# Kernel optimization log

Hardware: AMD Instinct MI355X
Metric: run time of the kernel (lower is better)

The kernel has to match this reference:

```python
import jax, jax.numpy as jnp
import numpy as np

D = 1024          # d_model
DFF_S = 2 * D     # memory/router FFN
DFF_E = 8 * D     # expert FFN
B = 1024          # batch
EPS = 1e-5
MEM_IDS = np.array([0, 2, 6, 8])    # corners: 'memory'
SMALL_IDS = np.array([0, 2, 4, 6, 8])  # dim_ff = 2*d (memory + router)
EXP_IDS = np.array([1, 3, 5, 7])    # edges: 'expert', dim_ff = 8*d

def _adjacency():
    A = np.zeros((9, 9), np.float32)
    for r in range(3):
        for c in range(3):
            i = r * 3 + c
            if r > 0: A[i, (r - 1) * 3 + c] = 1.0
            if r < 2: A[i, (r + 1) * 3 + c] = 1.0
            if c > 0: A[i, r * 3 + (c - 1)] = 1.0
            if c < 2: A[i, r * 3 + (c + 1)] = 1.0
    return A

def _ln(x, s, b):
    # x: [9, B, 1, D]; s, b: [9, D] (per-node LayerNorm params)
    mu = jnp.mean(x, axis=-1, keepdims=True)
    var = jnp.mean(jnp.square(x - mu), axis=-1, keepdims=True)
    return (x - mu) * jax.lax.rsqrt(var + EPS) * s[:, None, None, :] + b[:, None, None, :]

def setup_inputs() -> dict:
    key = jax.random.key(0)
    ks = jax.random.split(key, 12)
    sc = 0.02
    inp = {
        'seed': jax.random.normal(ks[0], (B, 1, D), jnp.float32),
        'ln1_s': jnp.ones((9, D), jnp.float32),
        'ln1_b': jnp.zeros((9, D), jnp.float32),
        'v_w': sc * jax.random.normal(ks[1], (9, D, D), jnp.float32),
        'v_b': jnp.zeros((9, D), jnp.float32),
        'o_w': sc * jax.random.normal(ks[2], (9, D, D), jnp.float32),
        'o_b': jnp.zeros((9, D), jnp.float32),
        'ln2_s': jnp.ones((9, D), jnp.float32),
        'ln2_b': jnp.zeros((9, D), jnp.float32),
        'w1_s': sc * jax.random.normal(ks[3], (5, DFF_S, D), jnp.float32),
        'b1_s': jnp.zeros((5, DFF_S), jnp.float32),
        'w2_s': sc * jax.random.normal(ks[4], (5, D, DFF_S), jnp.float32),
        'b2_s': jnp.zeros((5, D), jnp.float32),
        'w1_e': sc * jax.random.normal(ks[5], (4, DFF_E, D), jnp.float32),
        'b1_e': jnp.zeros((4, DFF_E), jnp.float32),
        'w2_e': sc * jax.random.normal(ks[6], (4, D, DFF_E), jnp.float32),
        'b2_e': jnp.zeros((4, D), jnp.float32),
        'steps': 3,
    }
    return inp

def reference(seed, ln1_s, ln1_b, v_w, v_b, o_w, o_b, ln2_s, ln2_b,
              w1_s, b1_s, w2_s, b2_s, w1_e, b1_e, w2_e, b2_e, steps):
    b = seed.shape[0]
    A = jnp.asarray(_adjacency(), seed.dtype)           # [9, 9] static grid topology
    S = jnp.zeros((9, b, 1, D), seed.dtype).at[4].set(seed)  # center = router = seed
    mem = jnp.zeros((4, b, 1, D), seed.dtype)           # memory-node hidden buffers
    mids = jnp.asarray(MEM_IDS)
    sids = jnp.asarray(SMALL_IDS)
    eids = jnp.asarray(EXP_IDS)
    for _ in range(steps):
        # neighbor sum over static 3x3 grid topology
        integ = jnp.einsum('mn,nbtd->mbtd', A, S)
        xn = _ln(integ, ln1_s, ln1_b)
        # seq_len == 1 => softmax over one key is 1 => attn = out_proj(v_proj(xn))
        v = jnp.einsum('nij,nbtj->nbti', v_w, xn) + v_b[:, None, None, :]
        attn = jnp.einsum('nij,nbtj->nbti', o_w, v) + o_b[:, None, None, :]
        x = integ + attn
        # memory nodes: new_memory = 0.7*mem + 0.3*x; x <- new_memory; buffer detached
        new_mem = 0.7 * mem + 0.3 * x[mids]
        x = x.at[mids].set(new_mem)
        mem = jax.lax.stop_gradient(new_mem)
        xn2 = _ln(x, ln2_s, ln2_b)
        # per-role MLPs (ReLU FFN)
        hs = jax.nn.relu(jnp.einsum('nfj,nbtj->nbtf', w1_s, xn2[sids]) + b1_s[:, None, None, :])
        outs = jnp.einsum('njf,nbtf->nbtj', w2_s, hs) + b2_s[:, None, None, :]
        he = jax.nn.relu(jnp.einsum('nfj,nbtj->nbtf', w1_e, xn2[eids]) + b1_e[:, None, None, :])
        oute = jnp.einsum('njf,nbtf->nbtj', w2_e, he) + b2_e[:, None, None, :]
        S = x.at[sids].add(outs).at[eids].add(oute)
    return S  # [9, B, 1, D] = final grid states
```

## Files before the change

### kernel.cpp

```cpp
#include <hip/hip_runtime.h>

#define BD (1024LL * 1024LL)

using bf16x8 = __attribute__((ext_vector_type(8))) __bf16;
using f32x4  = __attribute__((ext_vector_type(4))) float;

__device__ __forceinline__ unsigned short f2bf(float f) {
  unsigned int u = __float_as_uint(f);
  u += 0x7fffu + ((u >> 16) & 1u);
  return (unsigned short)(u >> 16);
}
__device__ __forceinline__ float bf2f(unsigned short h) {
  return __uint_as_float((unsigned int)h << 16);
}

__device__ __forceinline__ void gl_lds16(const unsigned short* g, unsigned short* l) {
  __builtin_amdgcn_global_load_lds(
      (const __attribute__((address_space(1))) void*)g,
      (__attribute__((address_space(3))) void*)l, 16, 0, 0);
}

__global__ __launch_bounds__(256) void cvt_kernel(const float* __restrict__ src,
                                                  unsigned short* __restrict__ dst,
                                                  long long n4) {
  long long i = (long long)blockIdx.x * 256 + threadIdx.x;
  if (i >= n4) return;
  float4 v = *(const float4*)(src + i * 4);
  unsigned int lo = (unsigned int)f2bf(v.x) | ((unsigned int)f2bf(v.y) << 16);
  unsigned int hi = (unsigned int)f2bf(v.z) | ((unsigned int)f2bf(v.w) << 16);
  *(uint2*)(dst + i * 4) = make_uint2(lo, hi);
}

__global__ __launch_bounds__(256) void tcvt_kernel(const float* __restrict__ src,
                                                   unsigned short* __restrict__ dst) {
  __shared__ float tile[32][33];
  const int n = blockIdx.z;
  const int bk = blockIdx.y * 32;
  const int bj = blockIdx.x * 32;
  const int tx = threadIdx.x & 31;
  const int ty = threadIdx.x >> 5;
#pragma unroll
  for (int r = 0; r < 4; ++r)
    tile[ty + r * 8][tx] = src[(long long)n * BD + (long long)(bk + ty + r * 8) * 1024 + bj + tx];
  __syncthreads();
#pragma unroll
  for (int r = 0; r < 4; ++r)
    dst[(long long)n * BD + (long long)(bj + ty + r * 8) * 1024 + bk + tx] =
        f2bf(tile[tx][ty + r * 8]);
}

__global__ __launch_bounds__(256) void cb_kernel(const float* __restrict__ o_w,
                                                 const float* __restrict__ v_b,
                                                 const float* __restrict__ o_b,
                                                 float* __restrict__ cb) {
  const int n = blockIdx.y;
  const int i = blockIdx.x * 4 + (threadIdx.x >> 6);
  const int lane = threadIdx.x & 63;
  const float* row = o_w + (long long)n * BD + (long long)i * 1024;
  const float* vb = v_b + n * 1024;
  float s = 0.f;
#pragma unroll
  for (int t = 0; t < 16; ++t) s += row[lane + t * 64] * vb[lane + t * 64];
  for (int off = 32; off > 0; off >>= 1) s += __shfl_down(s, off);
  if (lane == 0) cb[n * 1024 + i] = o_b[n * 1024 + i] + s;
}

__global__ __launch_bounds__(256) void init_kernel(const float* __restrict__ seed,
                                                   float* __restrict__ S,
                                                   float* __restrict__ mem) {
  long long i = (long long)blockIdx.x * 256 + threadIdx.x;
  const long long S4 = 9 * BD / 4;
  if (i < S4) {
    float4 v = make_float4(0.f, 0.f, 0.f, 0.f);
    const long long lo4 = 4 * BD / 4, hi4 = 5 * BD / 4;
    if (i >= lo4 && i < hi4) v = *(const float4*)(seed + (i - lo4) * 4);
    *(float4*)(S + i * 4) = v;
  } else {
    long long j = i - S4;
    *(float4*)(mem + j * 4) = make_float4(0.f, 0.f, 0.f, 0.f);
  }
}

template <bool ADJ>
__global__ __launch_bounds__(256) void ln_kernel(const float* __restrict__ in,
                                                 const float* __restrict__ gam,
                                                 const float* __restrict__ bet,
                                                 float* __restrict__ integ,
                                                 unsigned short* __restrict__ out) {
  const int row = blockIdx.x;
  const int node = blockIdx.y;
  const int tid = threadIdx.x;
  const long long rowoff = (long long)row * 1024 + tid * 4;
  const long long base = (long long)node * BD + rowoff;
  float4 v;
  if (ADJ) {
    v = make_float4(0.f, 0.f, 0.f, 0.f);
    const int r = node / 3, c = node % 3;
    if (r > 0) { float4 t = *(const float4*)(in + (node - 3) * BD + rowoff); v.x += t.x; v.y += t.y; v.z += t.z; v.w += t.w; }
    if (r < 2) { float4 t = *(const float4*)(in + (node + 3) * BD + rowoff); v.x += t.x; v.y += t.y; v.z += t.z; v.w += t.w; }
    if (c > 0) { float4 t = *(const float4*)(in + (node - 1) * BD + rowoff); v.x += t.x; v.y += t.y; v.z += t.z; v.w += t.w; }
    if (c < 2) { float4 t = *(const float4*)(in + (node + 1) * BD + rowoff); v.x += t.x; v.y += t.y; v.z += t.z; v.w += t.w; }
    *(float4*)(integ + base) = v;
  } else {
    v = *(const float4*)(in + base);
  }
  float s = v.x + v.y + v.z + v.w;
  float q = v.x * v.x + v.y * v.y + v.z * v.z + v.w * v.w;
  for (int off = 32; off > 0; off >>= 1) {
    s += __shfl_down(s, off);
    q += __shfl_down(q, off);
  }
  __shared__ float red[8];
  if ((tid & 63) == 0) { red[tid >> 6] = s; red[4 + (tid >> 6)] = q; }
  __syncthreads();
  s = red[0] + red[1] + red[2] + red[3];
  q = red[4] + red[5] + red[6] + red[7];
  const float mean = s * (1.0f / 1024.0f);
  const float var = q * (1.0f / 1024.0f) - mean * mean;
  const float inv = rsqrtf(var + 1e-5f);
  const float4 g = *(const float4*)(gam + node * 1024 + tid * 4);
  const float4 b = *(const float4*)(bet + node * 1024 + tid * 4);
  const float o0 = (v.x - mean) * inv * g.x + b.x;
  const float o1 = (v.y - mean) * inv * g.y + b.y;
  const float o2 = (v.z - mean) * inv * g.z + b.z;
  const float o3 = (v.w - mean) * inv * g.w + b.w;
  unsigned int lo = (unsigned int)f2bf(o0) | ((unsigned int)f2bf(o1) << 16);
  unsigned int hi = (unsigned int)f2bf(o2) | ((unsigned int)f2bf(o3) << 16);
  *(uint2*)(out + base) = make_uint2(lo, hi);
}

template <int MODE>
__global__ __launch_bounds__(256, 3) void gemm_kernel(
    const unsigned short* __restrict__ X, long long sX,
    const unsigned short* __restrict__ W, long long sW,
    const float* __restrict__ bias, int sBias,
    const float* __restrict__ add, long long sAdd,
    float* __restrict__ memio,
    void* __restrict__ outp, long long sOut,
    int N, int K, int SK) {
  __shared__ unsigned short Als[128 * 32];
  __shared__ unsigned short Bls[128 * 32];
  const int z = blockIdx.z;
  const int node = z / SK;
  const int kz = z - node * SK;
  const int Kper = K / SK;
  const int kbeg = kz * Kper;
  const long long bm = (long long)blockIdx.y * 128;
  const long long bn = (long long)blockIdx.x * 128;
  const unsigned short* Xz = X + (long long)node * sX;
  const unsigned short* Wz = W + (long long)node * sW;
  const int tid = threadIdx.x;
  const int lane = tid & 63;
  const int wid = tid >> 6;
  const int wm = (wid >> 1) * 64;
  const int wn = (wid & 1) * 64;
  const int lm = lane & 15;
  const int quad = lane >> 4;

  f32x4 acc[4][4] = {};

  const int lrow = lane >> 2;
  const int gch = ((lane & 3) ^ ((lane >> 3) & 3)) * 8;
  const int fch = (quad ^ ((lm >> 1) & 3)) * 8;

  for (int k0 = kbeg; k0 < kbeg + Kper; k0 += 32) {
    __syncthreads();
#pragma unroll
    for (int t = 0; t < 2; ++t) {
      const int idx = wid * 2 + t;
      const long long row = idx * 16 + lrow;
      gl_lds16(Xz + (bm + row) * K + k0 + gch, &Als[idx * 512]);
      gl_lds16(Wz + (bn + row) * K + k0 + gch, &Bls[idx * 512]);
    }
    __syncthreads();
    bf16x8 af[4], bfv[4];
#pragma unroll
    for (int i = 0; i < 4; ++i)
      af[i] = *(const bf16x8*)&Als[(wm + i * 16 + lm) * 32 + fch];
#pragma unroll
    for (int j = 0; j < 4; ++j)
      bfv[j] = *(const bf16x8*)&Bls[(wn + j * 16 + lm) * 32 + fch];
#pragma unroll
    for (int i = 0; i < 4; ++i)
#pragma unroll
      for (int j = 0; j < 4; ++j)
        acc[i][j] = __builtin_amdgcn_mfma_f32_16x16x32_bf16(af[i], bfv[j], acc[i][j], 0, 0, 0);
  }

  if (MODE == 4) {
    unsigned short* out = (unsigned short*)outp + (long long)z * sOut;
#pragma unroll
    for (int i = 0; i < 4; ++i) {
      const long long rb = bm + wm + i * 16 + quad * 4;
#pragma unroll
      for (int j = 0; j < 4; ++j) {
        const int col = (int)bn + wn + j * 16 + lm;
#pragma unroll
        for (int r = 0; r < 4; ++r)
          out[(rb + r) * (long long)N + col] = f2bf(acc[i][j][r]);
      }
    }
  } else {
    const float* bz = bias + (long long)node * sBias;
    float* out = (float*)outp + (long long)node * sOut;
    const float* az = add + (long long)node * sAdd;
    const bool is_mem = (node != 4) && ((node & 1) == 0);
    float* mz = nullptr;
    if (is_mem) {
      const int mi = (node == 0) ? 0 : (node == 2) ? 1 : (node == 6) ? 2 : 3;
      mz = memio + (long long)mi * BD;
    }
#pragma unroll
    for (int i = 0; i < 4; ++i) {
      const long long rb = bm + wm + i * 16 + quad * 4;
#pragma unroll
      for (int j = 0; j < 4; ++j) {
        const int col = (int)bn + wn + j * 16 + lm;
        const float bv = bz[col];
#pragma unroll
        for (int r = 0; r < 4; ++r) {
          const long long idx = (rb + r) * (long long)N + col;
          float v = acc[i][j][r] + bv + az[idx];
          if (is_mem) {
            v = 0.7f * mz[idx] + 0.3f * v;
            mz[idx] = v;
          }
          out[idx] = v;
        }
      }
    }
  }
}

template <int MODE>
__global__ __launch_bounds__(512, 2) void gemm256_kernel(
    const unsigned short* __restrict__ X, long long sX,
    const unsigned short* __restrict__ W, long long sW,
    const float* __restrict__ bias, int sBias,
    void* __restrict__ outp, long long sOut,
    int N, int K, int SK) {
  __shared__ __attribute__((aligned(16))) unsigned short lds[2][2][2][8192];
  const int z = blockIdx.z;
  const int node = z / SK;
  const int kz = z - node * SK;
  const int Kper = K / SK;
  const int kbeg = kz * Kper;
  const long long bm = (long long)blockIdx.y * 256;
  const long long bn = (long long)blockIdx.x * 256;
  const unsigned short* Xz = X + (long long)node * sX;
  const unsigned short* Wz = W + (long long)node * sW;
  const int tid = threadIdx.x;
  const int lane = tid & 63;
  const int wid = tid >> 6;
  const int wrow = (wid >> 2) * 128;
  const int wcol = (wid & 3) * 64;
  const int lm = lane & 15;
  const int quad = lane >> 4;
  const int lrow = lane >> 2;
  const int gch = ((lane & 3) ^ ((lane >> 3) & 3)) * 8;
  const int fch = (quad ^ ((lm >> 1) & 3)) * 8;

  f32x4 acc[8][4] = {};
  bf16x8 af[4][2], bfv[4][2];

  const int GA = (wid & 3) + ((wid >> 2) << 3);
  const int GB = ((wid >> 1) << 2) + (wid & 1);
  const unsigned short* pA[2] = {
      Xz + (bm + (long long)GA * 16 + lrow) * K + gch,
      Xz + (bm + (long long)(GA + 4) * 16 + lrow) * K + gch };
  const unsigned short* pB[2] = {
      Wz + (bn + (long long)GB * 16 + lrow) * K + gch,
      Wz + (bn + (long long)(GB + 2) * 16 + lrow) * K + gch };
  const int dA[2] = { GA * 512, (GA + 4) * 512 };
  const int dB[2] = { GB * 512, (GB + 2) * 512 };

  auto stageA = [&](int buf, int t, int hi) {
    const unsigned short* g = pA[hi] + kbeg + (long long)t * 64;
    gl_lds16(g,      &lds[buf][0][0][dA[hi]]);
    gl_lds16(g + 32, &lds[buf][0][1][dA[hi]]);
  };
  auto stageB = [&](int buf, int t, int hi) {
    const unsigned short* g = pB[hi] + kbeg + (long long)t * 64;
    gl_lds16(g,      &lds[buf][1][0][dB[hi]]);
    gl_lds16(g + 32, &lds[buf][1][1][dB[hi]]);
  };

#define LDA_HALF(BUF, IH)                                                      \
  _Pragma("unroll") for (int i_ = 0; i_ < 4; ++i_)                             \
      _Pragma("unroll") for (int k_ = 0; k_ < 2; ++k_)                         \
          af[i_][k_] = *(const bf16x8*)&lds[BUF][0][k_]                        \
              [(wrow + (IH) * 64 + i_ * 16 + lm) * 32 + fch];

#define LDB_HALF(BUF, JH)                                                      \
  _Pragma("unroll") for (int j_ = 0; j_ < 2; ++j_)                             \
      _Pragma("unroll") for (int k_ = 0; k_ < 2; ++k_)                         \
          bfv[(JH) * 2 + j_][k_] = *(const bf16x8*)&lds[BUF][1][k_]            \
              [(wcol + (JH) * 32 + j_ * 16 + lm) * 32 + fch];

#define MFMA_Q(IH, JH)                                                         \
  _Pragma("unroll") for (int i_ = 0; i_ < 4; ++i_)                             \
      _Pragma("unroll") for (int j_ = 0; j_ < 2; ++j_)                         \
          _Pragma("unroll") for (int k_ = 0; k_ < 2; ++k_)                     \
              acc[(IH) * 4 + i_][(JH) * 2 + j_] =                              \
                  __builtin_amdgcn_mfma_f32_16x16x32_bf16(                     \
                      af[i_][k_], bfv[(JH) * 2 + j_][k_],                      \
                      acc[(IH) * 4 + i_][(JH) * 2 + j_], 0, 0, 0);

#define PH_MID()                                          \
  __builtin_amdgcn_s_barrier();                           \
  asm volatile("s_waitcnt lgkmcnt(0)" ::: "memory");      \
  __builtin_amdgcn_s_setprio(1);

#define PH_END()                                          \
  __builtin_amdgcn_s_setprio(0);                          \
  __builtin_amdgcn_s_barrier();

  const int NIT = Kper >> 7;

  stageA(0, 0, 0); stageB(0, 0, 0); stageB(0, 0, 1); stageA(0, 0, 1);
  stageA(1, 1, 0); stageB(1, 1, 0); stageB(1, 1, 1);
  asm volatile("s_waitcnt vmcnt(6)" ::: "memory");
  __builtin_amdgcn_s_barrier();

#pragma unroll 1
  for (int I = 0; I < NIT; ++I) {
    const bool notlast = (I + 1 < NIT);
    const int t0 = 2 * I;
    LDA_HALF(0, 0) LDB_HALF(0, 0)
    stageA(1, t0 + 1, 1);
    PH_MID() MFMA_Q(0, 0) PH_END()
    LDB_HALF(0, 1)
    if (notlast) stageA(0, t0 + 2, 0);
    PH_MID() MFMA_Q(0, 1) PH_END()
    LDA_HALF(0, 1)
    if (notlast) stageB(0, t0 + 2, 0);
    PH_MID() MFMA_Q(1, 0) PH_END()
    if (notlast) stageB(0, t0 + 2, 1);
    PH_MID() MFMA_Q(1, 1)
    __builtin_amdgcn_s_setprio(0);
    if (notlast) asm volatile("s_waitcnt vmcnt(6)" ::: "memory");
    else         asm volatile("s_waitcnt vmcnt(0)" ::: "memory");
    __builtin_amdgcn_s_barrier();
    LDA_HALF(1, 0) LDB_HALF(1, 0)
    if (notlast) stageA(0, t0 + 2, 1);
    PH_MID() MFMA_Q(0, 0) PH_END()
    LDB_HALF(1, 1)
    if (notlast) stageA(1, t0 + 3, 0);
    PH_MID() MFMA_Q(0, 1) PH_END()
    LDA_HALF(1, 1)
    if (notlast) stageB(1, t0 + 3, 0);
    PH_MID() MFMA_Q(1, 0) PH_END()
    if (notlast) stageB(1, t0 + 3, 1);
    PH_MID() MFMA_Q(1, 1)
    __builtin_amdgcn_s_setprio(0);
    if (notlast) asm volatile("s_waitcnt vmcnt(6)" ::: "memory");
    __builtin_amdgcn_s_barrier();
  }

  if (MODE == 2) {
    const float* bz = bias + (long long)node * sBias;
    unsigned short* out = (unsigned short*)outp + (long long)node * sOut;
#pragma unroll
    for (int i = 0; i < 8; ++i) {
      const long long rb = bm + wrow + i * 16 + quad * 4;
#pragma unroll
      for (int j = 0; j < 4; ++j) {
        const int col = (int)bn + wcol + j * 16 + lm;
        const float bv = bz[col];
#pragma unroll
        for (int r = 0; r < 4; ++r)
          out[(rb + r) * (long long)N + col] = f2bf(fmaxf(acc[i][j][r] + bv, 0.0f));
      }
    }
  } else {
    unsigned short* out = (unsigned short*)outp + (long long)z * sOut;
#pragma unroll
    for (int i = 0; i < 8; ++i) {
      const long long rb = bm + wrow + i * 16 + quad * 4;
#pragma unroll
      for (int j = 0; j < 4; ++j) {
        const int col = (int)bn + wcol + j * 16 + lm;
#pragma unroll
        for (int r = 0; r < 4; ++r)
          out[(rb + r) * (long long)N + col] = f2bf(acc[i][j][r]);
      }
    }
  }
#undef LDA_HALF
#undef LDB_HALF
#undef MFMA_Q
#undef PH_MID
#undef PH_END
}

__global__ __launch_bounds__(256) void reduce_kernel(const unsigned short* __restrict__ part_s,
                                                     const unsigned short* __restrict__ part_e,
                                                     const float* __restrict__ b2s,
                                                     const float* __restrict__ b2e,
                                                     float* __restrict__ S) {
  const int node = blockIdx.y;
  const long long i8 = ((long long)blockIdx.x * 256 + threadIdx.x) * 8;
  const int col = (int)(i8 & 1023);
  const unsigned short* base;
  const float* bias;
  int SKn;
  if (node & 1) {
    const int e = (node - 1) >> 1;
    base = part_e + (long long)(e * 4) * BD + i8;
    bias = b2e + e * 1024;
    SKn = 4;
  } else {
    const int si = node >> 1;
    base = part_s + (long long)(si * 2) * BD + i8;
    bias = b2s + si * 1024;
    SKn = 2;
  }
  float sum[8] = {};
  for (int kz = 0; kz < SKn; ++kz) {
    uint4 p = *(const uint4*)(base + (long long)kz * BD);
    const unsigned short* ph = (const unsigned short*)&p;
#pragma unroll
    for (int j = 0; j < 8; ++j) sum[j] += bf2f(ph[j]);
  }
  float* sp = S + (long long)node * BD + i8;
  float4 s0 = *(float4*)sp;
  float4 s1 = *(float4*)(sp + 4);
  s0.x += sum[0] + bias[col + 0];
  s0.y += sum[1] + bias[col + 1];
  s0.z += sum[2] + bias[col + 2];
  s0.w += sum[3] + bias[col + 3];
  s1.x += sum[4] + bias[col + 4];
  s1.y += sum[5] + bias[col + 5];
  s1.z += sum[6] + bias[col + 6];
  s1.w += sum[7] + bias[col + 7];
  *(float4*)sp = s0;
  *(float4*)(sp + 4) = s1;
}

extern "C" void kernel_launch(void* const* d_in, const int* in_sizes, int n_in,
                              void* d_out, int out_size, void* d_ws, size_t ws_size,
                              hipStream_t stream) {
  const float* seed  = (const float*)d_in[0];
  const float* ln1_s = (const float*)d_in[1];
  const float* ln1_b = (const float*)d_in[2];
  const float* v_w   = (const float*)d_in[3];
  const float* v_b   = (const float*)d_in[4];
  const float* o_w   = (const float*)d_in[5];
  const float* o_b   = (const float*)d_in[6];
  const float* ln2_s = (const float*)d_in[7];
  const float* ln2_b = (const float*)d_in[8];
  const float* w1_s  = (const float*)d_in[9];
  const float* b1_s  = (const float*)d_in[10];
  const float* w2_s  = (const float*)d_in[11];
  const float* b2_s  = (const float*)d_in[12];
  const float* w1_e  = (const float*)d_in[13];
  const float* b1_e  = (const float*)d_in[14];
  const float* w2_e  = (const float*)d_in[15];
  const float* b2_e  = (const float*)d_in[16];

  char* ws = (char*)d_ws;
  size_t off = 0;
  auto alloc = [&](long long elems, int esize) {
    void* p = ws + off;
    off += (size_t)((elems * esize + 255LL) & ~255LL);
    return p;
  };
  unsigned short* wo    = (unsigned short*)alloc(9 * BD, 2);
  unsigned short* vwT   = (unsigned short*)alloc(9 * BD, 2);
  unsigned short* wc    = (unsigned short*)alloc(9 * BD, 2);
  unsigned short* w1s   = (unsigned short*)alloc(10 * BD, 2);
  unsigned short* w2s   = (unsigned short*)alloc(10 * BD, 2);
  unsigned short* w1e   = (unsigned short*)alloc(32 * BD, 2);
  unsigned short* w2e   = (unsigned short*)alloc(32 * BD, 2);
  float*          membuf= (float*)alloc(4 * BD, 4);
  float*          cb    = (float*)alloc(9 * 1024, 4);
  char* region = (char*)alloc(9 * BD * 4 + 9 * BD * 2, 1);
  float*          integ  = (float*)region;
  unsigned short* xn     = (unsigned short*)(region + 9 * BD * 4);
  unsigned short* part_s = (unsigned short*)region;
  unsigned short* part_e = (unsigned short*)(region + 10 * BD * 2);
  unsigned short* hs    = (unsigned short*)alloc(10 * BD, 2);
  unsigned short* he    = (unsigned short*)alloc(32 * BD, 2);

  float* S = (float*)d_out;

  cvt_kernel<<<(unsigned)(9  * BD / 1024), 256, 0, stream>>>(o_w,  wo,  9  * BD / 4);
  tcvt_kernel<<<dim3(32, 32, 9), 256, 0, stream>>>(v_w, vwT);
  cvt_kernel<<<(unsigned)(10 * BD / 1024), 256, 0, stream>>>(w1_s, w1s, 10 * BD / 4);
  cvt_kernel<<<(unsigned)(10 * BD / 1024), 256, 0, stream>>>(w2_s, w2s, 10 * BD / 4);
  cvt_kernel<<<(unsigned)(32 * BD / 1024), 256, 0, stream>>>(w1_e, w1e, 32 * BD / 4);
  cvt_kernel<<<(unsigned)(32 * BD / 1024), 256, 0, stream>>>(w2_e, w2e, 32 * BD / 4);
  cb_kernel<<<dim3(256, 9), 256, 0, stream>>>(o_w, v_b, o_b, cb);
  gemm_kernel<4><<<dim3(8, 8, 9), 256, 0, stream>>>(
      wo, BD, vwT, BD, nullptr, 0, nullptr, 0, nullptr, (void*)wc, BD, 1024, 1024, 1);
  init_kernel<<<(unsigned)(13 * BD / 1024), 256, 0, stream>>>(seed, S, membuf);

  for (int step = 0; step < 3; ++step) {
    ln_kernel<true><<<dim3(1024, 9), 256, 0, stream>>>(S, ln1_s, ln1_b, integ, xn);
    gemm_kernel<1><<<dim3(8, 8, 9), 256, 0, stream>>>(
        xn, BD, wc, BD, cb, 1024, integ, BD, membuf, (void*)S, BD, 1024, 1024, 1);
    ln_kernel<false><<<dim3(1024, 9), 256, 0, stream>>>(S, ln2_s, ln2_b, nullptr, xn);
    gemm256_kernel<2><<<dim3(8, 4, 5), 512, 0, stream>>>(
        xn, 2 * BD, w1s, 2 * BD, b1_s, 2048, (void*)hs, 2 * BD, 2048, 1024, 1);
    gemm256_kernel<2><<<dim3(32, 4, 4), 512, 0, stream>>>(
        xn + BD, 2 * BD, w1e, 8 * BD, b1_e, 8192, (void*)he, 8 * BD, 8192, 1024, 1);
    gemm256_kernel<4><<<dim3(4, 4, 10), 512, 0, stream>>>(
        hs, 2 * BD, w2s, 2 * BD, nullptr, 0, (void*)part_s, BD, 1024, 2048, 2);
    gemm256_kernel<4><<<dim3(4, 4, 16), 512, 0, stream>>>(
        he, 8 * BD, w2e, 8 * BD, nullptr, 0, (void*)part_e, BD, 1024, 8192, 4);
    reduce_kernel<<<dim3(512, 9), 256, 0, stream>>>(part_s, part_e, b2_s, b2_e, S);
  }
}
```

Baseline: 1.509 ms.

## Use 256-tile GEMM for attention and fuse residual/memory update with LN2

Replaces the 128-tile attention GEMM, which had a fused float epilogue, with the 256-tile GEMM that writes bf16 output to a scratch buffer aliased onto he. A new combine kernel then adds integ, the bf16 attention output and the combined bias, applies the memory blend, writes S and computes LayerNorm2 into xn in one pass. This drops the separate LN2 kernel's re-read of S and moves the GEMM to a larger tile. In exchange it adds a bf16 round-trip of the attention output before the residual add, which costs precision, and the 9x16 grid gives only 144 blocks.

New measurement: 1.396 ms. 7.5% less time.

```diff
diff --git a/kernel.cpp b/kernel.cpp
--- a/kernel.cpp
+++ b/kernel.cpp
@@ -129,107 +129,64 @@
   *(uint2*)(out + base) = make_uint2(lo, hi);
 }
 
-template <int MODE>
-__global__ __launch_bounds__(256, 3) void gemm_kernel(
-    const unsigned short* __restrict__ X, long long sX,
-    const unsigned short* __restrict__ W, long long sW,
-    const float* __restrict__ bias, int sBias,
-    const float* __restrict__ add, long long sAdd,
-    float* __restrict__ memio,
-    void* __restrict__ outp, long long sOut,
-    int N, int K, int SK) {
-  __shared__ unsigned short Als[128 * 32];
-  __shared__ unsigned short Bls[128 * 32];
-  const int z = blockIdx.z;
-  const int node = z / SK;
-  const int kz = z - node * SK;
-  const int Kper = K / SK;
-  const int kbeg = kz * Kper;
-  const long long bm = (long long)blockIdx.y * 128;
-  const long long bn = (long long)blockIdx.x * 128;
-  const unsigned short* Xz = X + (long long)node * sX;
-  const unsigned short* Wz = W + (long long)node * sW;
+__global__ __launch_bounds__(256) void combine_kernel(
+    const float* __restrict__ integ,
+    const unsigned short* __restrict__ attn,
+    const float* __restrict__ cb,
+    const float* __restrict__ gam, const float* __restrict__ bet,
+    float* __restrict__ membuf,
+    float* __restrict__ S,
+    unsigned short* __restrict__ xn2) {
+  const int row = blockIdx.x;
+  const int node = blockIdx.y;
   const int tid = threadIdx.x;
-  const int lane = tid & 63;
-  const int wid = tid >> 6;
-  const int wm = (wid >> 1) * 64;
-  const int wn = (wid & 1) * 64;
-  const int lm = lane & 15;
-  const int quad = lane >> 4;
-
-  f32x4 acc[4][4] = {};
-
-  const int lrow = lane >> 2;
-  const int gch = ((lane & 3) ^ ((lane >> 3) & 3)) * 8;
-  const int fch = (quad ^ ((lm >> 1) & 3)) * 8;
-
-  for (int k0 = kbeg; k0 < kbeg + Kper; k0 += 32) {
-    __syncthreads();
-#pragma unroll
-    for (int t = 0; t < 2; ++t) {
-      const int idx = wid * 2 + t;
-      const long long row = idx * 16 + lrow;
-      gl_lds16(Xz + (bm + row) * K + k0 + gch, &Als[idx * 512]);
-      gl_lds16(Wz + (bn + row) * K + k0 + gch, &Bls[idx * 512]);
-    }
-    __syncthreads();
-    bf16x8 af[4], bfv[4];
-#pragma unroll
-    for (int i = 0; i < 4; ++i)
-      af[i] = *(const bf16x8*)&Als[(wm + i * 16 + lm) * 32 + fch];
-#pragma unroll
-    for (int j = 0; j < 4; ++j)
-      bfv[j] = *(const bf16x8*)&Bls[(wn + j * 16 + lm) * 32 + fch];
-#pragma unroll
-    for (int i = 0; i < 4; ++i)
-#pragma unroll
-      for (int j = 0; j < 4; ++j)
-        acc[i][j] = __builtin_amdgcn_mfma_f32_16x16x32_bf16(af[i], bfv[j], acc[i][j], 0, 0, 0);
-  }
-
-  if (MODE == 4) {
-    unsigned short* out = (unsigned short*)outp + (long long)z * sOut;
-#pragma unroll
-    for (int i = 0; i < 4; ++i) {
-      const long long rb = bm + wm + i * 16 + quad * 4;
-#pragma unroll
-      for (int j = 0; j < 4; ++j) {
-        const int col = (int)bn + wn + j * 16 + lm;
-#pragma unroll
-        for (int r = 0; r < 4; ++r)
-          out[(rb + r) * (long long)N + col] = f2bf(acc[i][j][r]);
-      }
-    }
-  } else {
-    const float* bz = bias + (long long)node * sBias;
-    float* out = (float*)outp + (long long)node * sOut;
-    const float* az = add + (long long)node * sAdd;
-    const bool is_mem = (node != 4) && ((node & 1) == 0);
-    float* mz = nullptr;
-    if (is_mem) {
-      const int mi = (node == 0) ? 0 : (node == 2) ? 1 : (node == 6) ? 2 : 3;
-      mz = memio + (long long)mi * BD;
-    }
-#pragma unroll
-    for (int i = 0; i < 4; ++i) {
-      const long long rb = bm + wm + i * 16 + quad * 4;
-#pragma unroll
-      for (int j = 0; j < 4; ++j) {
-        const int col = (int)bn + wn + j * 16 + lm;
-        const float bv = bz[col];
-#pragma unroll
-        for (int r = 0; r < 4; ++r) {
-          const long long idx = (rb + r) * (long long)N + col;
-          float v = acc[i][j][r] + bv + az[idx];
-          if (is_mem) {
-            v = 0.7f * mz[idx] + 0.3f * v;
-            mz[idx] = v;
-          }
-          out[idx] = v;
-        }
-      }
-    }
-  }
+  const long long rowoff = (long long)row * 1024 + tid * 4;
+  const long long base = (long long)node * BD + rowoff;
+
+  float4 v = *(const float4*)(integ + base);
+  const uint2 a = *(const uint2*)(attn + base);
+  const float4 c = *(const float4*)(cb + node * 1024 + tid * 4);
+  v.x += bf2f((unsigned short)(a.x & 0xffffu)) + c.x;
+  v.y += bf2f((unsigned short)(a.x >> 16)) + c.y;
+  v.z += bf2f((unsigned short)(a.y & 0xffffu)) + c.z;
+  v.w += bf2f((unsigned short)(a.y >> 16)) + c.w;
+
+  const bool is_mem = (node != 4) && ((node & 1) == 0);
+  if (is_mem) {
+    const int mi = (node == 0) ? 0 : (node == 2) ? 1 : (node == 6) ? 2 : 3;
+    float* mz = membuf + (long long)mi * BD + rowoff;
+    const float4 m = *(const float4*)mz;
+    v.x = 0.7f * m.x + 0.3f * v.x;
+    v.y = 0.7f * m.y + 0.3f * v.y;
+    v.z = 0.7f * m.z + 0.3f * v.z;
+    v.w = 0.7f * m.w + 0.3f * v.w;
+    *(float4*)mz = v;
+  }
+  *(float4*)(S + base) = v;
+
+  float s = v.x + v.y + v.z + v.w;
+  float q = v.x * v.x + v.y * v.y + v.z * v.z + v.w * v.w;
+  for (int off = 32; off > 0; off >>= 1) {
+    s += __shfl_down(s, off);
+    q += __shfl_down(q, off);
+  }
+  __shared__ float red[8];
+  if ((tid & 63) == 0) { red[tid >> 6] = s; red[4 + (tid >> 6)] = q; }
+  __syncthreads();
+  s = red[0] + red[1] + red[2] + red[3];
+  q = red[4] + red[5] + red[6] + red[7];
+  const float mean = s * (1.0f / 1024.0f);
+  const float var = q * (1.0f / 1024.0f) - mean * mean;
+  const float inv = rsqrtf(var + 1e-5f);
+  const float4 g = *(const float4*)(gam + node * 1024 + tid * 4);
+  const float4 b = *(const float4*)(bet + node * 1024 + tid * 4);
+  const float o0 = (v.x - mean) * inv * g.x + b.x;
+  const float o1 = (v.y - mean) * inv * g.y + b.y;
+  const float o2 = (v.z - mean) * inv * g.z + b.z;
+  const float o3 = (v.w - mean) * inv * g.w + b.w;
+  unsigned int lo = (unsigned int)f2bf(o0) | ((unsigned int)f2bf(o1) << 16);
+  unsigned int hi = (unsigned int)f2bf(o2) | ((unsigned int)f2bf(o3) << 16);
+  *(uint2*)(xn2 + base) = make_uint2(lo, hi);
 }
 
 template <int MODE>
@@ -481,6 +438,7 @@
   unsigned short* part_e = (unsigned short*)(region + 10 * BD * 2);
   unsigned short* hs    = (unsigned short*)alloc(10 * BD, 2);
   unsigned short* he    = (unsigned short*)alloc(32 * BD, 2);
+  unsigned short* att_p = he;
 
   float* S = (float*)d_out;
 
@@ -491,15 +449,16 @@
   cvt_kernel<<<(unsigned)(32 * BD / 1024), 256, 0, stream>>>(w1_e, w1e, 32 * BD / 4);
   cvt_kernel<<<(unsigned)(32 * BD / 1024), 256, 0, stream>>>(w2_e, w2e, 32 * BD / 4);
   cb_kernel<<<dim3(256, 9), 256, 0, stream>>>(o_w, v_b, o_b, cb);
-  gemm_kernel<4><<<dim3(8, 8, 9), 256, 0, stream>>>(
-      wo, BD, vwT, BD, nullptr, 0, nullptr, 0, nullptr, (void*)wc, BD, 1024, 1024, 1);
+  gemm256_kernel<4><<<dim3(4, 4, 9), 512, 0, stream>>>(
+      wo, BD, vwT, BD, nullptr, 0, (void*)wc, BD, 1024, 1024, 1);
   init_kernel<<<(unsigned)(13 * BD / 1024), 256, 0, stream>>>(seed, S, membuf);
 
   for (int step = 0; step < 3; ++step) {
     ln_kernel<true><<<dim3(1024, 9), 256, 0, stream>>>(S, ln1_s, ln1_b, integ, xn);
-    gemm_kernel<1><<<dim3(8, 8, 9), 256, 0, stream>>>(
-        xn, BD, wc, BD, cb, 1024, integ, BD, membuf, (void*)S, BD, 1024, 1024, 1);
-    ln_kernel<false><<<dim3(1024, 9), 256, 0, stream>>>(S, ln2_s, ln2_b, nullptr, xn);
+    gemm256_kernel<4><<<dim3(4, 4, 9), 512, 0, stream>>>(
+        xn, BD, wc, BD, nullptr, 0, (void*)att_p, BD, 1024, 1024, 1);
+    combine_kernel<<<dim3(1024, 9), 256, 0, stream>>>(
+        integ, att_p, cb, ln2_s, ln2_b, membuf, S, xn);
     gemm256_kernel<2><<<dim3(8, 4, 5), 512, 0, stream>>>(
         xn, 2 * BD, w1s, 2 * BD, b1_s, 2048, (void*)hs, 2 * BD, 2048, 1024, 1);
     gemm256_kernel<2><<<dim3(32, 4, 4), 512, 0, stream>>>(
```
